# Kernel tuning notes

Hardware: AMD Instinct MI355X
Metric: run time of the kernel (lower is better)

## Reference

```python
import jax, jax.numpy as jnp
import numpy as np
from jax import lax

B, L, D, H, FF, NL, MAXLEN = 8, 2048, 512, 8, 2048, 2, 8000
DK = D // H
EPS = 1e-5


def _ln(x, g, b):
    m = x.mean(-1, keepdims=True)
    v = ((x - m) ** 2).mean(-1, keepdims=True)
    return (x - m) * lax.rsqrt(v + EPS) * g + b


def setup_inputs() -> dict:
    key = jax.random.key(0)
    ks = jax.random.split(key, 24)
    s = 0.02
    inp = {
        "x": jax.random.normal(ks[0], (B, 1, L), jnp.float32),
        "conv_w": jax.random.normal(ks[1], (D, 1, 5), jnp.float32) * s,
        "conv_b": jnp.zeros((D,), jnp.float32),
        "gn_g": jnp.ones((D,), jnp.float32),
        "gn_b": jnp.zeros((D,), jnp.float32),
        "pe_k": jax.random.normal(ks[2], (2 * MAXLEN, DK), jnp.float32) * s,
        "ln1_g": jnp.ones((NL, D), jnp.float32),
        "ln1_b": jnp.zeros((NL, D), jnp.float32),
        "wq": jax.random.normal(ks[3], (NL, D, D), jnp.float32) * s,
        "bq": jnp.zeros((NL, D), jnp.float32),
        "wk": jax.random.normal(ks[4], (NL, D, D), jnp.float32) * s,
        "bk": jnp.zeros((NL, D), jnp.float32),
        "wv": jax.random.normal(ks[5], (NL, D, D), jnp.float32) * s,
        "bv": jnp.zeros((NL, D), jnp.float32),
        "wo": jax.random.normal(ks[6], (NL, D, D), jnp.float32) * s,
        "bo": jnp.zeros((NL, D), jnp.float32),
        "lscale": jnp.full((NL, D), 1e-5, jnp.float32),
        "ln2_g": jnp.ones((NL, D), jnp.float32),
        "ln2_b": jnp.zeros((NL, D), jnp.float32),
        "w1": jax.random.normal(ks[7], (NL, D, FF), jnp.float32) * s,
        "b1": jnp.zeros((NL, FF), jnp.float32),
        "w2": jax.random.normal(ks[8], (NL, FF, D), jnp.float32) * s,
        "b2": jnp.zeros((NL, D), jnp.float32),
    }
    return inp


def reference(x, conv_w, conv_b, gn_g, gn_b, pe_k, ln1_g, ln1_b, wq, bq, wk, bk,
              wv, bv, wo, bo, lscale, ln2_g, ln2_b, w1, b1, w2, b2):
    # frontend: Conv1d(1, D, k=5, s=2, p=2) + ReLU + GroupNorm(1, D)
    h = lax.conv_general_dilated(x, conv_w, (2,), [(2, 2)],
                                 dimension_numbers=("NCH", "OIH", "NCH"))
    h = jax.nn.relu(h + conv_b[None, :, None])
    m = h.mean((1, 2), keepdims=True)
    v = ((h - m) ** 2).mean((1, 2), keepdims=True)
    h = (h - m) * lax.rsqrt(v + EPS) * gn_g[None, :, None] + gn_b[None, :, None]
    h = h.transpose(0, 2, 1)  # (B, T, D)
    T = h.shape[1]

    # relative positional encoding: (T, T, DK) key bias table, clamped
    r = jnp.arange(T)
    rel = jnp.clip(r[None, :] - r[:, None], -MAXLEN, MAXLEN - 1) + MAXLEN
    pos_k = jnp.clip(pe_k[rel], -5.0, 5.0)  # (T, T, DK)

    inv_sqrt_dk = 1.0 / np.sqrt(DK).astype(np.float32)
    for i in range(NL):
        xn = _ln(h, ln1_g[i], ln1_b[i])
        q = (xn @ wq[i] + bq[i]).reshape(B, T, H, DK).transpose(0, 2, 1, 3)
        k = (xn @ wk[i] + bk[i]).reshape(B, T, H, DK).transpose(0, 2, 1, 3)
        vv = (xn @ wv[i] + bv[i]).reshape(B, T, H, DK).transpose(0, 2, 1, 3)
        scores = jnp.einsum("bhid,bhjd->bhij", q, k) * inv_sqrt_dk
        scores = scores + jnp.einsum("bhid,ijd->bhij", q, pos_k) * inv_sqrt_dk
        attn = jax.nn.softmax(scores, axis=-1)
        o = jnp.einsum("bhij,bhjd->bhid", attn, vv)
        o = o.transpose(0, 2, 1, 3).reshape(B, T, D)
        h = h + (o @ wo[i] + bo[i]) * lscale[i]
        # FFN with pre-norm
        hn = _ln(h, ln2_g[i], ln2_b[i])
        h = h + jax.nn.relu(hn @ w1[i] + b1[i]) @ w2[i] + b2[i]
    return h
```

## Files before the change

### kernel.cpp

```cpp
#include <hip/hip_runtime.h>


typedef unsigned short u16;
typedef __attribute__((ext_vector_type(8))) short bf16x8;
typedef __attribute__((ext_vector_type(4))) float f32x4;

#define GLD16(gp, lp) __builtin_amdgcn_global_load_lds( \
    (const __attribute__((address_space(1))) void*)(gp), \
    (__attribute__((address_space(3))) void*)(lp), 16, 0, 0)

__device__ __forceinline__ u16 f2bf(float f) {
  unsigned u = __float_as_uint(f);
  u += 0x7fffu + ((u >> 16) & 1u);
  return (u16)(u >> 16);
}
__device__ __forceinline__ float bf2f(u16 s) {
  return __uint_as_float(((unsigned)s) << 16);
}

__global__ __launch_bounds__(256) void conv_front(
    const float* __restrict__ x, const float* __restrict__ cw,
    const float* __restrict__ cb, float* __restrict__ out) {
  int idx = blockIdx.x * 256 + threadIdx.x;
  int c = idx & 511;
  int bt = idx >> 9;
  int t = bt & 1023;
  int b = bt >> 10;
  const float* xp = x + b * 2048;
  float acc = cb[c];
#pragma unroll
  for (int k = 0; k < 5; ++k) {
    int xi = 2 * t + k - 2;
    float xv = (xi >= 0 && xi < 2048) ? xp[xi] : 0.f;
    acc = fmaf(xv, cw[c * 5 + k], acc);
  }
  out[idx] = fmaxf(acc, 0.f);
}

__global__ __launch_bounds__(256) void gn_stats(
    const float* __restrict__ conv, float* __restrict__ stats) {
  int b = blockIdx.y;
  const float* p = conv + (size_t)b * 524288 + blockIdx.x * 8192;
  float s = 0.f, q = 0.f;
#pragma unroll
  for (int i = 0; i < 8; ++i) {
    float4 v = *(const float4*)(p + i * 1024 + threadIdx.x * 4);
    s += v.x + v.y + v.z + v.w;
    q += v.x * v.x + v.y * v.y + v.z * v.z + v.w * v.w;
  }
#pragma unroll
  for (int d = 1; d < 64; d <<= 1) { s += __shfl_xor(s, d); q += __shfl_xor(q, d); }
  if ((threadIdx.x & 63) == 0) {
    atomicAdd(&stats[b * 2], s);
    atomicAdd(&stats[b * 2 + 1], q);
  }
}

__global__ __launch_bounds__(256) void gn_ln(
    const float* __restrict__ conv, const float* __restrict__ stats,
    const float* __restrict__ gng, const float* __restrict__ gnb,
    const float* __restrict__ lng, const float* __restrict__ lnb,
    float* __restrict__ h, u16* __restrict__ xn) {
  const int row = blockIdx.x * 4 + (threadIdx.x >> 6);
  const int l = threadIdx.x & 63;
  const int b = row >> 10;
  float gm = stats[b * 2] * (1.f / 524288.f);
  float gv = stats[b * 2 + 1] * (1.f / 524288.f) - gm * gm;
  float grs = rsqrtf(gv + 1e-5f);
  const float* p = conv + (size_t)row * 512 + l * 8;
  float4 a4 = *(const float4*)p;
  float4 b4 = *(const float4*)(p + 4);
  float v[8] = {a4.x, a4.y, a4.z, a4.w, b4.x, b4.y, b4.z, b4.w};
#pragma unroll
  for (int e = 0; e < 8; ++e) {
    int c = l * 8 + e;
    v[e] = (v[e] - gm) * grs * gng[c] + gnb[c];
  }
  float* hp = h + (size_t)row * 512 + l * 8;
  *(float4*)hp = make_float4(v[0], v[1], v[2], v[3]);
  *(float4*)(hp + 4) = make_float4(v[4], v[5], v[6], v[7]);
  float s = 0.f, q = 0.f;
#pragma unroll
  for (int e = 0; e < 8; ++e) { s += v[e]; q += v[e] * v[e]; }
#pragma unroll
  for (int d = 1; d < 64; d <<= 1) { s += __shfl_xor(s, d); q += __shfl_xor(q, d); }
  float mean = s * (1.f / 512.f);
  float rs = rsqrtf(q * (1.f / 512.f) - mean * mean + 1e-5f);
  bf16x8 ov;
#pragma unroll
  for (int e = 0; e < 8; ++e) {
    int c = l * 8 + e;
    ov[e] = (short)f2bf((v[e] - mean) * rs * lng[c] + lnb[c]);
  }
  *(bf16x8*)(xn + (size_t)row * 512 + l * 8) = ov;
}

__global__ __launch_bounds__(256) void ln_rows(
    const float* __restrict__ in, const float* __restrict__ gg,
    const float* __restrict__ bb, u16* __restrict__ out) {
  const int row = blockIdx.x * 4 + (threadIdx.x >> 6);
  const int l = threadIdx.x & 63;
  const float* p = in + (size_t)row * 512 + l * 8;
  float4 a4 = *(const float4*)p;
  float4 b4 = *(const float4*)(p + 4);
  float v[8] = {a4.x, a4.y, a4.z, a4.w, b4.x, b4.y, b4.z, b4.w};
  float s = 0.f, q = 0.f;
#pragma unroll
  for (int e = 0; e < 8; ++e) { s += v[e]; q += v[e] * v[e]; }
#pragma unroll
  for (int d = 1; d < 64; d <<= 1) { s += __shfl_xor(s, d); q += __shfl_xor(q, d); }
  float mean = s * (1.f / 512.f);
  float rs = rsqrtf(q * (1.f / 512.f) - mean * mean + 1e-5f);
  bf16x8 ov;
#pragma unroll
  for (int e = 0; e < 8; ++e) {
    int c = l * 8 + e;
    ov[e] = (short)f2bf((v[e] - mean) * rs * gg[c] + bb[c]);
  }
  *(bf16x8*)(out + (size_t)row * 512 + l * 8) = ov;
}

__global__ __launch_bounds__(256) void cvt_wt(
    const float* __restrict__ src, u16* __restrict__ dst, int N, int kshift,
    size_t src_lstride, size_t dst_lstride) {
  src += blockIdx.y * src_lstride;
  dst += blockIdx.y * dst_lstride;
  int idx = blockIdx.x * 256 + threadIdx.x;
  int K = 1 << kshift;
  int n = idx >> kshift;
  int k = idx & (K - 1);
  if (n >= N) return;
  dst[idx] = f2bf(src[(size_t)k * N + n]);
}

__global__ void pack_qkv_bias(const float* __restrict__ bq, const float* __restrict__ bk,
                              const float* __restrict__ bv, float* __restrict__ dst) {
  int lyr = blockIdx.y;
  int i = blockIdx.x * 256 + threadIdx.x;
  if (i < 512) dst[lyr * 1536 + i] = bq[lyr * 512 + i];
  else if (i < 1024) dst[lyr * 1536 + i] = bk[lyr * 512 + i - 512];
  else if (i < 1536) dst[lyr * 1536 + i] = bv[lyr * 512 + i - 1024];
}

__global__ void cvt_pk(const float* __restrict__ pe, u16* __restrict__ pkb) {
  int i = blockIdx.x * 256 + threadIdx.x;
  if (i >= 2047 * 64) return;
  float v = pe[i + 6977 * 64];
  v = fminf(fmaxf(v, -5.f), 5.f);
  pkb[i] = f2bf(v);
}

__global__ __launch_bounds__(256) void transpV(
    const u16* __restrict__ qkv, u16* __restrict__ vT) {
  __shared__ short tile[64][72];
  const int tid = threadIdx.x;
  const int tt = blockIdx.x, bh = blockIdx.y;
  const int b = bh >> 3, h = bh & 7;
#pragma unroll
  for (int rr = 0; rr < 2; ++rr) {
    int trow = rr * 32 + (tid >> 3);
    bf16x8 v = *(const bf16x8*)(qkv + (size_t)(b * 1024 + tt * 64 + trow) * 1536 +
                                1024 + h * 64 + (tid & 7) * 8);
#pragma unroll
    for (int e = 0; e < 8; ++e) tile[trow][(tid & 7) * 8 + e] = v[e];
  }
  __syncthreads();
#pragma unroll
  for (int rr = 0; rr < 2; ++rr) {
    int d = rr * 32 + (tid >> 3);
    bf16x8 ov;
#pragma unroll
    for (int e = 0; e < 8; ++e) ov[e] = tile[(tid & 7) * 8 + e][d];
    *(bf16x8*)(vT + ((size_t)bh * 64 + d) * 1024 + tt * 64 + (tid & 7) * 8) = ov;
  }
}

template <int EPI>
__global__ __launch_bounds__(256) void gemm128(
    const u16* __restrict__ A, const u16* __restrict__ Wt,
    const float* __restrict__ bias, const float* __restrict__ scl,
    const float* __restrict__ resid, float* __restrict__ outf,
    u16* __restrict__ outb, int N, int K) {
  __shared__ __attribute__((aligned(16))) u16 As[2][128 * 32];
  __shared__ __attribute__((aligned(16))) u16 Bs[2][128 * 32];
  const int tid = threadIdx.x;
  const int l = tid & 63, w = tid >> 6;
  const int g = l >> 4, r = l & 15;
  const int wr = w >> 1, wc = w & 1;
  const int m0 = blockIdx.y * 128, n0 = blockIdx.x * 128;

  const f32x4 fz = {0.f, 0.f, 0.f, 0.f};
  f32x4 acc[4][4];
#pragma unroll
  for (int i = 0; i < 4; ++i)
#pragma unroll
    for (int j = 0; j < 4; ++j) acc[i][j] = fz;

  const int nkt = K >> 5;
  const int arow = tid >> 2, acol = (tid & 3) * 8;
  const u16* aG = A + (size_t)(m0 + arow) * K + acol;
  const u16* bG = Wt + (size_t)(n0 + arow) * K + acol;

  auto stage = [&](int kt, int buf) {
    const u16* ga = aG + kt * 32;
    const u16* gb = bG + kt * 32;
    u16* la = &As[buf][tid * 8];
    u16* lb = &Bs[buf][tid * 8];
    GLD16(ga, la);
    GLD16(ga + (size_t)64 * K, la + 2048);
    GLD16(gb, lb);
    GLD16(gb + (size_t)64 * K, lb + 2048);
  };

  stage(0, 0);
  __syncthreads();
  for (int kt = 0; kt < nkt; ++kt) {
    const int cb = kt & 1;
    if (kt + 1 < nkt) stage(kt + 1, cb ^ 1);
    bf16x8 af[4], bfr[4];
#pragma unroll
    for (int mi = 0; mi < 4; ++mi)
      af[mi] = *(const bf16x8*)&As[cb][(wr * 64 + mi * 16 + r) * 32 + g * 8];
#pragma unroll
    for (int ni = 0; ni < 4; ++ni)
      bfr[ni] = *(const bf16x8*)&Bs[cb][(wc * 64 + ni * 16 + r) * 32 + g * 8];
#pragma unroll
    for (int mi = 0; mi < 4; ++mi)
#pragma unroll
      for (int ni = 0; ni < 4; ++ni)
        acc[mi][ni] = __builtin_amdgcn_mfma_f32_16x16x32_bf16(
            af[mi], bfr[ni], acc[mi][ni], 0, 0, 0);
    __syncthreads();
  }

#pragma unroll
  for (int mi = 0; mi < 4; ++mi)
#pragma unroll
    for (int ni = 0; ni < 4; ++ni)
#pragma unroll
      for (int reg = 0; reg < 4; ++reg) {
        int gm = m0 + wr * 64 + mi * 16 + g * 4 + reg;
        int gn = n0 + wc * 64 + ni * 16 + r;
        float v = acc[mi][ni][reg] + bias[gn];
        size_t oi = (size_t)gm * N + gn;
        if constexpr (EPI == 0) outb[oi] = f2bf(v);
        else if constexpr (EPI == 1) outb[oi] = f2bf(fmaxf(v, 0.f));
        else if constexpr (EPI == 2) outf[oi] = resid[oi] + v * scl[gn];
        else outf[oi] = resid[oi] + v;
      }
}

__global__ __launch_bounds__(256, 4) void attn64(
    const u16* __restrict__ qkv, const u16* __restrict__ vT,
    const u16* __restrict__ pkb, u16* __restrict__ o) {
  __shared__ __attribute__((aligned(16))) u16 lds[20480];
  u16* Kt   = lds;
  u16* Vtt  = lds + 4096;
  u16* PkMt = lds + 8192;
  u16* Pt   = lds + 16384;

  const int tid = threadIdx.x, l = tid & 63, w = tid >> 6;
  const int g = l >> 4, r = l & 15;
  const int iblk = blockIdx.x, bh = blockIdx.y;
  const int b = bh >> 3, h = bh & 7;
  const int i0 = iblk * 64;

  bf16x8 aq[2];
  {
    const u16* qp = qkv + (size_t)(b * 1024 + i0 + w * 16 + r) * 1536 + h * 64 + g * 8;
    aq[0] = *(const bf16x8*)(qp);
    aq[1] = *(const bf16x8*)(qp + 32);
  }

  const f32x4 fz = {0.f, 0.f, 0.f, 0.f};
  float mrow[4], lpart[4];
  f32x4 oacc[4];
#pragma unroll
  for (int i = 0; i < 4; ++i) { mrow[i] = -1e30f; lpart[i] = 0.f; oacc[i] = fz; }

  for (int jt = 0; jt < 16; ++jt) {
    const int j0 = jt * 64;
    {
      const u16* kg = qkv + (size_t)(b * 1024 + j0) * 1536 + 512 + h * 64;
      const u16* vg = vT + (size_t)bh * 64 * 1024 + j0;
      const int rbase = j0 - i0 + 960;
#pragma unroll
      for (int rr = 0; rr < 2; ++rr) {
        int row = rr * 32 + (tid >> 3);
        int colb = ((tid & 7) * 16) ^ ((row & 7) << 4);
        GLD16(kg + (size_t)row * 1536 + (colb >> 1), Kt + rr * 2048 + tid * 8);
        GLD16(vg + (size_t)row * 1024 + (colb >> 1), Vtt + rr * 2048 + tid * 8);
      }
#pragma unroll
      for (int rr = 0; rr < 4; ++rr) {
        int row = rr * 32 + (tid >> 3);
        int colb = ((tid & 7) * 16) ^ ((row & 7) << 4);
        int gr = rbase + row;
        gr = gr < 0 ? 0 : (gr > 2046 ? 2046 : gr);
        GLD16(pkb + (size_t)gr * 64 + (colb >> 1), PkMt + rr * 2048 + tid * 8);
      }
    }
    __syncthreads();

    f32x4 sacc[4];
#pragma unroll
    for (int cf = 0; cf < 4; ++cf) sacc[cf] = fz;
#pragma unroll
    for (int ks = 0; ks < 2; ++ks)
#pragma unroll
      for (int cf = 0; cf < 4; ++cf) {
        int row = cf * 16 + r;
        int colb = (ks * 64 + g * 16) ^ ((row & 7) << 4);
        bf16x8 bk = *(const bf16x8*)(Kt + row * 64 + (colb >> 1));
        sacc[cf] = __builtin_amdgcn_mfma_f32_16x16x32_bf16(aq[ks], bk, sacc[cf], 0, 0, 0);
      }

    f32x4 macc[8];
#pragma unroll
    for (int mf = 0; mf < 8; ++mf) {
      macc[mf] = fz;
#pragma unroll
      for (int ks = 0; ks < 2; ++ks) {
        int row = mf * 16 + r;
        int colb = (ks * 64 + g * 16) ^ ((row & 7) << 4);
        bf16x8 bp = *(const bf16x8*)(PkMt + row * 64 + (colb >> 1));
        macc[mf] = __builtin_amdgcn_mfma_f32_16x16x32_bf16(aq[ks], bp, macc[mf], 0, 0, 0);
      }
    }
    __syncthreads();

#pragma unroll
    for (int mf = 0; mf < 8; ++mf)
#pragma unroll
      for (int reg = 0; reg < 4; ++reg)
        PkMt[(w * 16 + g * 4 + reg) * 128 + mf * 16 + r] = f2bf(macc[mf][reg]);

    float sv[4][4], pmax[4];
#pragma unroll
    for (int reg = 0; reg < 4; ++reg) pmax[reg] = -1e30f;
#pragma unroll
    for (int cf = 0; cf < 4; ++cf)
#pragma unroll
      for (int reg = 0; reg < 4; ++reg) {
        int ii = w * 16 + g * 4 + reg;
        int jj = cf * 16 + r;
        float s = (sacc[cf][reg] + bf2f(PkMt[ii * 128 + jj - ii + 63])) * 0.125f;
        sv[cf][reg] = s;
        pmax[reg] = fmaxf(pmax[reg], s);
      }
#pragma unroll
    for (int d = 1; d < 16; d <<= 1)
#pragma unroll
      for (int reg = 0; reg < 4; ++reg)
        pmax[reg] = fmaxf(pmax[reg], __shfl_xor(pmax[reg], d));
#pragma unroll
    for (int reg = 0; reg < 4; ++reg) {
      float mnew = fmaxf(mrow[reg], pmax[reg]);
      float corr = __expf(mrow[reg] - mnew);
      mrow[reg] = mnew;
      lpart[reg] *= corr;
#pragma unroll
      for (int df = 0; df < 4; ++df) oacc[df][reg] *= corr;
      float ps = 0.f;
      int ii = w * 16 + g * 4 + reg;
#pragma unroll
      for (int cf = 0; cf < 4; ++cf) {
        float p = __expf(sv[cf][reg] - mnew);
        ps += p;
        int jj = cf * 16 + r;
        int colb = (jj * 2) ^ ((ii & 7) << 4);
        Pt[ii * 64 + (colb >> 1)] = f2bf(p);
      }
      lpart[reg] += ps;
    }

#pragma unroll
    for (int ks = 0; ks < 2; ++ks) {
      int prow = w * 16 + r;
      int pcolb = (ks * 64 + g * 16) ^ ((prow & 7) << 4);
      bf16x8 ap = *(const bf16x8*)(Pt + prow * 64 + (pcolb >> 1));
#pragma unroll
      for (int df = 0; df < 4; ++df) {
        int vrow = df * 16 + r;
        int vcolb = (ks * 64 + g * 16) ^ ((vrow & 7) << 4);
        bf16x8 bv = *(const bf16x8*)(Vtt + vrow * 64 + (vcolb >> 1));
        oacc[df] = __builtin_amdgcn_mfma_f32_16x16x32_bf16(ap, bv, oacc[df], 0, 0, 0);
      }
    }
    __syncthreads();
  }

#pragma unroll
  for (int d = 1; d < 16; d <<= 1)
#pragma unroll
    for (int reg = 0; reg < 4; ++reg) lpart[reg] += __shfl_xor(lpart[reg], d);
#pragma unroll
  for (int reg = 0; reg < 4; ++reg) {
    float inv = 1.f / lpart[reg];
    int ii = w * 16 + g * 4 + reg;
#pragma unroll
    for (int df = 0; df < 4; ++df)
      o[(size_t)(b * 1024 + i0 + ii) * 512 + h * 64 + df * 16 + r] =
          f2bf(oacc[df][reg] * inv);
  }
}

extern "C" void kernel_launch(void* const* d_in, const int* in_sizes, int n_in,
                              void* d_out, int out_size, void* d_ws, size_t ws_size,
                              hipStream_t stream) {
  (void)in_sizes; (void)n_in; (void)out_size;
  const float* x      = (const float*)d_in[0];
  const float* conv_w = (const float*)d_in[1];
  const float* conv_b = (const float*)d_in[2];
  const float* gn_g   = (const float*)d_in[3];
  const float* gn_b   = (const float*)d_in[4];
  const float* pe_k   = (const float*)d_in[5];
  const float* ln1_g  = (const float*)d_in[6];
  const float* ln1_b  = (const float*)d_in[7];
  const float* wq     = (const float*)d_in[8];
  const float* bq     = (const float*)d_in[9];
  const float* wk     = (const float*)d_in[10];
  const float* bk     = (const float*)d_in[11];
  const float* wv     = (const float*)d_in[12];
  const float* bv     = (const float*)d_in[13];
  const float* wo     = (const float*)d_in[14];
  const float* bo     = (const float*)d_in[15];
  const float* lsc    = (const float*)d_in[16];
  const float* ln2_g  = (const float*)d_in[17];
  const float* ln2_b  = (const float*)d_in[18];
  const float* w1     = (const float*)d_in[19];
  const float* b1     = (const float*)d_in[20];
  const float* w2     = (const float*)d_in[21];
  const float* b2     = (const float*)d_in[22];

  char* ws = (char*)d_ws;
  size_t off = 0;
  auto alloc = [&](size_t bytes) {
    char* p = ws + off;
    off = (off + bytes + 255) & ~(size_t)255;
    return p;
  };
  float* hbuf  = (float*)alloc((size_t)8192 * 512 * 4);
  u16* xn      = (u16*)alloc((size_t)8192 * 512 * 2);
  u16* qkvb    = (u16*)alloc((size_t)8192 * 1536 * 2);
  u16* vTb     = (u16*)alloc((size_t)64 * 64 * 1024 * 2);
  u16* ob      = (u16*)alloc((size_t)8192 * 512 * 2);
  u16* f1      = (u16*)alloc((size_t)8192 * 2048 * 2);
  float* stats = (float*)alloc(256);
  u16* wqkvb   = (u16*)alloc((size_t)2 * 1536 * 512 * 2);
  u16* wob     = (u16*)alloc((size_t)2 * 512 * 512 * 2);
  u16* w1b     = (u16*)alloc((size_t)2 * 2048 * 512 * 2);
  u16* w2b     = (u16*)alloc((size_t)2 * 512 * 2048 * 2);
  float* bqkv  = (float*)alloc(2 * 1536 * 4);
  u16* pkbuf   = (u16*)alloc(2047 * 64 * 2);
  if (off > ws_size) return;
  float* convb = (float*)f1;

  hipMemsetAsync(stats, 0, 64, stream);

  cvt_wt<<<dim3(1024, 2), 256, 0, stream>>>(wq, wqkvb, 512, 9, 262144, 786432);
  cvt_wt<<<dim3(1024, 2), 256, 0, stream>>>(wk, wqkvb + 262144, 512, 9, 262144, 786432);
  cvt_wt<<<dim3(1024, 2), 256, 0, stream>>>(wv, wqkvb + 524288, 512, 9, 262144, 786432);
  cvt_wt<<<dim3(1024, 2), 256, 0, stream>>>(wo, wob, 512, 9, 262144, 262144);
  cvt_wt<<<dim3(4096, 2), 256, 0, stream>>>(w1, w1b, 2048, 9, 1048576, 1048576);
  cvt_wt<<<dim3(4096, 2), 256, 0, stream>>>(w2, w2b, 512, 11, 1048576, 1048576);
  pack_qkv_bias<<<dim3(6, 2), 256, 0, stream>>>(bq, bk, bv, bqkv);
  cvt_pk<<<512, 256, 0, stream>>>(pe_k, pkbuf);

  conv_front<<<16384, 256, 0, stream>>>(x, conv_w, conv_b, convb);
  gn_stats<<<dim3(64, 8), 256, 0, stream>>>(convb, stats);
  gn_ln<<<2048, 256, 0, stream>>>(convb, stats, gn_g, gn_b, ln1_g, ln1_b, hbuf, xn);

  for (int lyr = 0; lyr < 2; ++lyr) {
    gemm128<0><<<dim3(12, 64), 256, 0, stream>>>(
        xn, wqkvb + (size_t)lyr * 786432, bqkv + lyr * 1536,
        nullptr, nullptr, nullptr, qkvb, 1536, 512);
    transpV<<<dim3(16, 64), 256, 0, stream>>>(qkvb, vTb);
    attn64<<<dim3(16, 64), 256, 0, stream>>>(qkvb, vTb, pkbuf, ob);
    gemm128<2><<<dim3(4, 64), 256, 0, stream>>>(
        ob, wob + (size_t)lyr * 262144, bo + lyr * 512,
        lsc + lyr * 512, hbuf, hbuf, nullptr, 512, 512);
    ln_rows<<<2048, 256, 0, stream>>>(hbuf, ln2_g + lyr * 512, ln2_b + lyr * 512, xn);
    gemm128<1><<<dim3(16, 64), 256, 0, stream>>>(
        xn, w1b + (size_t)lyr * 1048576, b1 + lyr * 2048,
        nullptr, nullptr, nullptr, f1, 2048, 512);
    float* outp = (lyr == 1) ? (float*)d_out : hbuf;
    gemm128<3><<<dim3(4, 64), 256, 0, stream>>>(
        f1, w2b + (size_t)lyr * 1048576, b2 + lyr * 512,
        nullptr, hbuf, outp, nullptr, 512, 2048);
    if (lyr == 0)
      ln_rows<<<2048, 256, 0, stream>>>(hbuf, ln1_g + 512, ln1_b + 512, xn);
  }
}
```

Baseline: 661.0 us.

## Reuse relative-position scores across key tiles and narrow N-tiles for D-output GEMMs

The attention kernel used to recompute a 128-wide band of q·pos_k products for every 64-key tile. It now computes only the new 64-wide half each tile and keeps the previous half in a second LDS buffer, which halves the positional MFMA work and the pe_k loads. The 1/sqrt(dk) scale is folded into the Q projection epilogue so the softmax loop no longer multiplies by it. The N=512 GEMMs (output projection and FFN2) use 64-wide N tiles so they launch twice as many blocks, trading some extra A-tile reloads for better CU occupancy.

```diff
diff --git a/kernel.cpp b/kernel.cpp
--- a/kernel.cpp
+++ b/kernel.cpp
@@ -175,26 +175,27 @@
   }
 }
 
-template <int EPI>
+template <int EPI, int BN>
 __global__ __launch_bounds__(256) void gemm128(
     const u16* __restrict__ A, const u16* __restrict__ Wt,
     const float* __restrict__ bias, const float* __restrict__ scl,
     const float* __restrict__ resid, float* __restrict__ outf,
     u16* __restrict__ outb, int N, int K) {
+  constexpr int NI = BN >> 5;
   __shared__ __attribute__((aligned(16))) u16 As[2][128 * 32];
-  __shared__ __attribute__((aligned(16))) u16 Bs[2][128 * 32];
+  __shared__ __attribute__((aligned(16))) u16 Bs[2][BN * 32];
   const int tid = threadIdx.x;
   const int l = tid & 63, w = tid >> 6;
   const int g = l >> 4, r = l & 15;
   const int wr = w >> 1, wc = w & 1;
-  const int m0 = blockIdx.y * 128, n0 = blockIdx.x * 128;
+  const int m0 = blockIdx.y * 128, n0 = blockIdx.x * BN;
 
   const f32x4 fz = {0.f, 0.f, 0.f, 0.f};
-  f32x4 acc[4][4];
+  f32x4 acc[4][NI];
 #pragma unroll
   for (int i = 0; i < 4; ++i)
 #pragma unroll
-    for (int j = 0; j < 4; ++j) acc[i][j] = fz;
+    for (int j = 0; j < NI; ++j) acc[i][j] = fz;
 
   const int nkt = K >> 5;
   const int arow = tid >> 2, acol = (tid & 3) * 8;
@@ -209,7 +210,7 @@
     GLD16(ga, la);
     GLD16(ga + (size_t)64 * K, la + 2048);
     GLD16(gb, lb);
-    GLD16(gb + (size_t)64 * K, lb + 2048);
+    if constexpr (BN == 128) GLD16(gb + (size_t)64 * K, lb + 2048);
   };
 
   stage(0, 0);
@@ -217,17 +218,17 @@
   for (int kt = 0; kt < nkt; ++kt) {
     const int cb = kt & 1;
     if (kt + 1 < nkt) stage(kt + 1, cb ^ 1);
-    bf16x8 af[4], bfr[4];
+    bf16x8 af[4], bfr[NI];
 #pragma unroll
     for (int mi = 0; mi < 4; ++mi)
       af[mi] = *(const bf16x8*)&As[cb][(wr * 64 + mi * 16 + r) * 32 + g * 8];
 #pragma unroll
-    for (int ni = 0; ni < 4; ++ni)
-      bfr[ni] = *(const bf16x8*)&Bs[cb][(wc * 64 + ni * 16 + r) * 32 + g * 8];
+    for (int ni = 0; ni < NI; ++ni)
+      bfr[ni] = *(const bf16x8*)&Bs[cb][(wc * (BN / 2) + ni * 16 + r) * 32 + g * 8];
 #pragma unroll
     for (int mi = 0; mi < 4; ++mi)
 #pragma unroll
-      for (int ni = 0; ni < 4; ++ni)
+      for (int ni = 0; ni < NI; ++ni)
         acc[mi][ni] = __builtin_amdgcn_mfma_f32_16x16x32_bf16(
             af[mi], bfr[ni], acc[mi][ni], 0, 0, 0);
     __syncthreads();
@@ -236,14 +237,14 @@
 #pragma unroll
   for (int mi = 0; mi < 4; ++mi)
 #pragma unroll
-    for (int ni = 0; ni < 4; ++ni)
+    for (int ni = 0; ni < NI; ++ni)
 #pragma unroll
       for (int reg = 0; reg < 4; ++reg) {
         int gm = m0 + wr * 64 + mi * 16 + g * 4 + reg;
-        int gn = n0 + wc * 64 + ni * 16 + r;
+        int gn = n0 + wc * (BN / 2) + ni * 16 + r;
         float v = acc[mi][ni][reg] + bias[gn];
         size_t oi = (size_t)gm * N + gn;
-        if constexpr (EPI == 0) outb[oi] = f2bf(v);
+        if constexpr (EPI == 0) outb[oi] = f2bf(gn < 512 ? v * 0.125f : v);
         else if constexpr (EPI == 1) outb[oi] = f2bf(fmaxf(v, 0.f));
         else if constexpr (EPI == 2) outf[oi] = resid[oi] + v * scl[gn];
         else outf[oi] = resid[oi] + v;
@@ -254,16 +255,19 @@
     const u16* __restrict__ qkv, const u16* __restrict__ vT,
     const u16* __restrict__ pkb, u16* __restrict__ o) {
   __shared__ __attribute__((aligned(16))) u16 lds[20480];
-  u16* Kt   = lds;
-  u16* Vtt  = lds + 4096;
-  u16* PkMt = lds + 8192;
-  u16* Pt   = lds + 16384;
+  u16* Kt  = lds;
+  u16* Vtt = lds + 4096;
+  u16* Rb0 = lds + 8192;
+  u16* Rb1 = lds + 12288;
+  u16* Pt  = lds + 16384;
 
   const int tid = threadIdx.x, l = tid & 63, w = tid >> 6;
   const int g = l >> 4, r = l & 15;
   const int iblk = blockIdx.x, bh = blockIdx.y;
   const int b = bh >> 3, h = bh & 7;
   const int i0 = iblk * 64;
+  const int relbase = 960 - i0;
+  const int iw = w * 16 + g * 4;
 
   bf16x8 aq[2];
   {
@@ -273,31 +277,59 @@
   }
 
   const f32x4 fz = {0.f, 0.f, 0.f, 0.f};
+
+  {
+#pragma unroll
+    for (int rr = 0; rr < 2; ++rr) {
+      int row = rr * 32 + (tid >> 3);
+      int colb = ((tid & 7) * 16) ^ ((row & 7) << 4);
+      int gr = relbase + row;
+      gr = gr > 2046 ? 2046 : gr;
+      GLD16(pkb + (size_t)gr * 64 + (colb >> 1), Rb0 + rr * 2048 + tid * 8);
+    }
+    __syncthreads();
+    f32x4 mac[4];
+#pragma unroll
+    for (int mf = 0; mf < 4; ++mf) {
+      mac[mf] = fz;
+#pragma unroll
+      for (int ks = 0; ks < 2; ++ks) {
+        int row = mf * 16 + r;
+        int colb = (ks * 64 + g * 16) ^ ((row & 7) << 4);
+        bf16x8 bp = *(const bf16x8*)(Rb0 + row * 64 + (colb >> 1));
+        mac[mf] = __builtin_amdgcn_mfma_f32_16x16x32_bf16(aq[ks], bp, mac[mf], 0, 0, 0);
+      }
+    }
+    __syncthreads();
+#pragma unroll
+    for (int mf = 0; mf < 4; ++mf)
+#pragma unroll
+      for (int reg = 0; reg < 4; ++reg)
+        Rb0[(iw + reg) * 64 + mf * 16 + r] = f2bf(mac[mf][reg]);
+  }
+
   float mrow[4], lpart[4];
   f32x4 oacc[4];
 #pragma unroll
   for (int i = 0; i < 4; ++i) { mrow[i] = -1e30f; lpart[i] = 0.f; oacc[i] = fz; }
 
   for (int jt = 0; jt < 16; ++jt) {
+    u16* Rcur  = (jt & 1) ? Rb0 : Rb1;
+    u16* Rprev = (jt & 1) ? Rb1 : Rb0;
     const int j0 = jt * 64;
     {
       const u16* kg = qkv + (size_t)(b * 1024 + j0) * 1536 + 512 + h * 64;
-      const u16* vg = vT + (size_t)bh * 64 * 1024 + j0;
-      const int rbase = j0 - i0 + 960;
+      const u16* vg = vT + (size_t)bh * 65536 + j0;
+      const int gbase = relbase + 64 * (jt + 1);
 #pragma unroll
       for (int rr = 0; rr < 2; ++rr) {
         int row = rr * 32 + (tid >> 3);
         int colb = ((tid & 7) * 16) ^ ((row & 7) << 4);
         GLD16(kg + (size_t)row * 1536 + (colb >> 1), Kt + rr * 2048 + tid * 8);
         GLD16(vg + (size_t)row * 1024 + (colb >> 1), Vtt + rr * 2048 + tid * 8);
-      }
-#pragma unroll
-      for (int rr = 0; rr < 4; ++rr) {
-        int row = rr * 32 + (tid >> 3);
-        int colb = ((tid & 7) * 16) ^ ((row & 7) << 4);
-        int gr = rbase + row;
-        gr = gr < 0 ? 0 : (gr > 2046 ? 2046 : gr);
-        GLD16(pkb + (size_t)gr * 64 + (colb >> 1), PkMt + rr * 2048 + tid * 8);
+        int gr = gbase + row;
+        gr = gr > 2046 ? 2046 : gr;
+        GLD16(pkb + (size_t)gr * 64 + (colb >> 1), Rcur + rr * 2048 + tid * 8);
       }
     }
     __syncthreads();
@@ -315,25 +347,25 @@
         sacc[cf] = __builtin_amdgcn_mfma_f32_16x16x32_bf16(aq[ks], bk, sacc[cf], 0, 0, 0);
       }
 
-    f32x4 macc[8];
-#pragma unroll
-    for (int mf = 0; mf < 8; ++mf) {
-      macc[mf] = fz;
+    f32x4 mac[4];
+#pragma unroll
+    for (int mf = 0; mf < 4; ++mf) {
+      mac[mf] = fz;
 #pragma unroll
       for (int ks = 0; ks < 2; ++ks) {
         int row = mf * 16 + r;
         int colb = (ks * 64 + g * 16) ^ ((row & 7) << 4);
-        bf16x8 bp = *(const bf16x8*)(PkMt + row * 64 + (colb >> 1));
-        macc[mf] = __builtin_amdgcn_mfma_f32_16x16x32_bf16(aq[ks], bp, macc[mf], 0, 0, 0);
+        bf16x8 bp = *(const bf16x8*)(Rcur + row * 64 + (colb >> 1));
+        mac[mf] = __builtin_amdgcn_mfma_f32_16x16x32_bf16(aq[ks], bp, mac[mf], 0, 0, 0);
       }
     }
     __syncthreads();
 
 #pragma unroll
-    for (int mf = 0; mf < 8; ++mf)
+    for (int mf = 0; mf < 4; ++mf)
 #pragma unroll
       for (int reg = 0; reg < 4; ++reg)
-        PkMt[(w * 16 + g * 4 + reg) * 128 + mf * 16 + r] = f2bf(macc[mf][reg]);
+        Rcur[(iw + reg) * 64 + mf * 16 + r] = f2bf(mac[mf][reg]);
 
     float sv[4][4], pmax[4];
 #pragma unroll
@@ -342,9 +374,11 @@
     for (int cf = 0; cf < 4; ++cf)
 #pragma unroll
       for (int reg = 0; reg < 4; ++reg) {
-        int ii = w * 16 + g * 4 + reg;
-        int jj = cf * 16 + r;
-        float s = (sacc[cf][reg] + bf2f(PkMt[ii * 128 + jj - ii + 63])) * 0.125f;
+        int iir = iw + reg;
+        int c63 = cf * 16 + r - iir + 63;
+        const u16* src = (c63 < 64) ? (Rprev + iir * 64 + c63)
+                                    : (Rcur + iir * 64 + c63 - 64);
+        float s = sacc[cf][reg] + bf2f(*src);
         sv[cf][reg] = s;
         pmax[reg] = fmaxf(pmax[reg], s);
       }
@@ -362,7 +396,7 @@
 #pragma unroll
       for (int df = 0; df < 4; ++df) oacc[df][reg] *= corr;
       float ps = 0.f;
-      int ii = w * 16 + g * 4 + reg;
+      int ii = iw + reg;
 #pragma unroll
       for (int cf = 0; cf < 4; ++cf) {
         float p = __expf(sv[cf][reg] - mnew);
@@ -397,7 +431,7 @@
 #pragma unroll
   for (int reg = 0; reg < 4; ++reg) {
     float inv = 1.f / lpart[reg];
-    int ii = w * 16 + g * 4 + reg;
+    int ii = iw + reg;
 #pragma unroll
     for (int df = 0; df < 4; ++df)
       o[(size_t)(b * 1024 + i0 + ii) * 512 + h * 64 + df * 16 + r] =
@@ -472,20 +506,20 @@
   gn_ln<<<2048, 256, 0, stream>>>(convb, stats, gn_g, gn_b, ln1_g, ln1_b, hbuf, xn);
 
   for (int lyr = 0; lyr < 2; ++lyr) {
-    gemm128<0><<<dim3(12, 64), 256, 0, stream>>>(
+    gemm128<0, 128><<<dim3(12, 64), 256, 0, stream>>>(
         xn, wqkvb + (size_t)lyr * 786432, bqkv + lyr * 1536,
         nullptr, nullptr, nullptr, qkvb, 1536, 512);
     transpV<<<dim3(16, 64), 256, 0, stream>>>(qkvb, vTb);
     attn64<<<dim3(16, 64), 256, 0, stream>>>(qkvb, vTb, pkbuf, ob);
-    gemm128<2><<<dim3(4, 64), 256, 0, stream>>>(
+    gemm128<2, 64><<<dim3(8, 64), 256, 0, stream>>>(
         ob, wob + (size_t)lyr * 262144, bo + lyr * 512,
         lsc + lyr * 512, hbuf, hbuf, nullptr, 512, 512);
     ln_rows<<<2048, 256, 0, stream>>>(hbuf, ln2_g + lyr * 512, ln2_b + lyr * 512, xn);
-    gemm128<1><<<dim3(16, 64), 256, 0, stream>>>(
+    gemm128<1, 128><<<dim3(16, 64), 256, 0, stream>>>(
         xn, w1b + (size_t)lyr * 1048576, b1 + lyr * 2048,
         nullptr, nullptr, nullptr, f1, 2048, 512);
     float* outp = (lyr == 1) ? (float*)d_out : hbuf;
-    gemm128<3><<<dim3(4, 64), 256, 0, stream>>>(
+    gemm128<3, 64><<<dim3(8, 64), 256, 0, stream>>>(
         f1, w2b + (size_t)lyr * 1048576, b2 + lyr * 512,
         nullptr, hbuf, outp, nullptr, 512, 2048);
     if (lyr == 0)
```

Result: faster. 625.1 us (-5.4%).
